# Performance work log

Hardware: AMD Instinct MI355X
Metric: run time of the kernel (lower is better)

Reference implementation:

```python
import jax, jax.numpy as jnp
import numpy as np

B, C, H, W = 2, 192, 128, 128
DG, K = 4, 9  # deformable groups, kernel taps (3x3)


def conv3x3(x, w, b):
    y = jax.lax.conv_general_dilated(x, w, (1, 1), ((1, 1), (1, 1)),
                                     dimension_numbers=('NCHW', 'OIHW', 'NCHW'))
    return y + b[None, :, None, None]


def deform_sample(x, dy, dx, mask):
    # x: [B,C,H,W]; dy,dx,mask: [B,DG,K,H,W]. Returns [B,C,K,H,W] masked bilinear samples.
    b, c, h, w = x.shape
    cg = c // DG
    kk = jnp.arange(K)
    ky = (kk // 3 - 1).astype(x.dtype)  # kernel row offsets {-1,0,1}, pad=1, stride=1
    kx = (kk % 3 - 1).astype(x.dtype)
    ii = jnp.arange(h, dtype=x.dtype)
    jj = jnp.arange(w, dtype=x.dtype)
    py = ii[None, None, None, :, None] + ky[None, None, :, None, None] + dy  # [B,DG,K,H,W]
    px = jj[None, None, None, None, :] + kx[None, None, :, None, None] + dx
    y0 = jnp.floor(py)
    x0 = jnp.floor(px)
    ly = py - y0
    lx = px - x0
    xf = x.reshape(b, DG, cg, h * w)
    out = jnp.zeros((b, DG, cg, K, h, w), dtype=x.dtype)
    corners = [(y0, x0, (1 - ly) * (1 - lx)), (y0, x0 + 1, (1 - ly) * lx),
               (y0 + 1, x0, ly * (1 - lx)), (y0 + 1, x0 + 1, ly * lx)]
    for yc, xc, wt in corners:
        valid = (yc >= 0) & (yc < h) & (xc >= 0) & (xc < w)  # zero padding outside
        wv = wt * valid.astype(x.dtype)
        idx = (jnp.clip(yc, 0, h - 1) * w + jnp.clip(xc, 0, w - 1)).astype(jnp.int32)
        idxb = jnp.broadcast_to(idx.reshape(b, DG, 1, K * h * w), (b, DG, cg, K * h * w))
        g = jnp.take_along_axis(xf, idxb, axis=3).reshape(b, DG, cg, K, h, w)
        out = out + wv[:, :, None] * g
    out = out * mask[:, :, None]
    return out.reshape(b, c, K, h, w)


def setup_inputs() -> dict:
    key = jax.random.key(0)
    ks = jax.random.split(key, 8)
    f32 = jnp.float32
    x_vq = jax.random.normal(ks[0], (B, C, H, W), f32)
    x_residual = jax.random.normal(ks[1], (B, C, H, W), f32)
    w_off = jax.random.normal(ks[2], (C, 2 * C, 3, 3), f32) * (1.0 / np.sqrt(2 * C * 9))
    b_off = jnp.zeros((C,), f32)
    # conv_offset of DCNv2Pack: C -> 3*DG*K channels; small init keeps offsets moderate
    w_co = jax.random.normal(ks[3], (3 * DG * K, C, 3, 3), f32) * 0.02
    b_co = jnp.zeros((3 * DG * K,), f32)
    w_dcn = jax.random.normal(ks[4], (C, C, 3, 3), f32) * (1.0 / np.sqrt(C * 9))
    b_dcn = jnp.zeros((C,), f32)
    return {"x_vq": x_vq, "x_residual": x_residual, "w_off": w_off, "b_off": b_off,
            "w_co": w_co, "b_co": b_co, "w_dcn": w_dcn, "b_dcn": b_dcn}


def reference(x_vq, x_residual, w_off, b_off, w_co, b_co, w_dcn, b_dcn):
    feat = conv3x3(jnp.concatenate([x_vq, x_residual], axis=1), w_off, b_off)  # [B,C,H,W]
    off_out = conv3x3(feat, w_co, b_co)  # [B,3*DG*K,H,W]
    gk = DG * K
    o1 = off_out[:, :gk]
    o2 = off_out[:, gk:2 * gk]
    mask = jax.nn.sigmoid(off_out[:, 2 * gk:])
    dy = o1.reshape(B, DG, K, H, W)
    dx = o2.reshape(B, DG, K, H, W)
    m = mask.reshape(B, DG, K, H, W)
    sampled = deform_sample(x_vq, dy, dx, m)  # [B,C,K,H,W]
    y = jnp.einsum('ock,bckhw->bohw', w_dcn.reshape(C, C, K), sampled)
    return y + b_dcn[None, :, None, None]
```

## Files before the change

### kernel.cpp

```cpp
#include <hip/hip_runtime.h>
#include <hip/hip_bf16.h>
#include <math.h>

#define HH 128
#define WW 128
#define HW 16384
#define BB 2
#define CC 192

typedef __attribute__((ext_vector_type(8)))  short short8;
typedef __attribute__((ext_vector_type(4)))  float f32x4;
typedef __attribute__((ext_vector_type(16))) float f32x16;
typedef __attribute__((ext_vector_type(2)))  float f32x2;
typedef __attribute__((ext_vector_type(4)))  unsigned u32x4;

static __device__ __forceinline__ short f2bf(float f) {
    unsigned u = __float_as_uint(f);
    unsigned r = (u + 0x7FFFu + ((u >> 16) & 1u)) >> 16;
    return (short)r;
}
static __device__ __forceinline__ f32x2 unpk(unsigned u) {
    f32x2 r;
    r[0] = __uint_as_float(u << 16);
    r[1] = __uint_as_float(u & 0xFFFF0000u);
    return r;
}

static __device__ __forceinline__ void gl_lds16(const short* gsrc, short* ldst) {
    __builtin_amdgcn_global_load_lds(
        (const __attribute__((address_space(1))) unsigned*)gsrc,
        (__attribute__((address_space(3))) unsigned*)ldst, 16, 0, 0);
}

__global__ __launch_bounds__(256) void to_grp_k(
    const float* __restrict__ xv, const float* __restrict__ xr,
    unsigned short* __restrict__ xg)
{
    const int idx = blockIdx.x * 256 + threadIdx.x;
    const int pos = idx & (HW - 1);
    const int cgb = idx >> 14;
    const int cg  = cgb % 48;
    const int b   = cgb / 48;
    short8 v;
#pragma unroll
    for (int r = 0; r < 8; r++) {
        const int c = cg * 8 + r;
        const float f = (c < 192)
            ? xv[((size_t)(b * 192 + c) << 14) + pos]
            : xr[((size_t)(b * 192 + (c - 192)) << 14) + pos];
        v[r] = f2bf(f);
    }
    *reinterpret_cast<short8*>(xg + (size_t)idx * 8) = v;
}

__global__ void pack_w_k(const float* __restrict__ w, short* __restrict__ wp,
                         int Co, int so, int d1, int s1, int d2, int s2, int s3,
                         int total)
{
    const int idx = blockIdx.x * blockDim.x + threadIdx.x;
    if (idx >= total) return;
    const int lane  = idx & 63;
    const int slot  = (idx >> 6) & 7;
    const int chunk = idx >> 9;
    const int o     = slot * 32 + (lane & 31);
    const int k0    = chunk * 16 + ((lane >> 5) << 3);
    short8 v;
#pragma unroll
    for (int r = 0; r < 8; r++) {
        const int k = k0 + r;
        float f = 0.f;
        if (o < Co) {
            const int rem = k % d1;
            f = w[(size_t)o * so + (k / d1) * s1 + (rem / d2) * s2 + (rem % d2) * s3];
        }
        v[r] = f2bf(f);
    }
    *reinterpret_cast<short8*>(wp + (size_t)idx * 8) = v;
}

template<int MTW, int NC16, bool OUT_GRP>
__global__ __launch_bounds__(256, 2) void conv_g_k(
    const unsigned short* __restrict__ xg,
    const short* __restrict__ wA, const float* __restrict__ bias,
    void* __restrict__ outp, int Cout)
{
    __shared__ __align__(16) short Pbuf[3][2][4096];

    const int t    = threadIdx.x;
    const int lane = t & 63;
    const int wid  = t >> 6;
    const int mg   = wid >> 1;
    const int nt   = wid & 1;
    const int lin  = (blockIdx.z * HH + blockIdx.y) * 2 + blockIdx.x;
    const int og_  = (lin & 7) * 64 + (lin >> 3);
    const int j0   = (og_ & 1) * 64;
    const int i    = (og_ >> 1) & (HH - 1);
    const int b    = og_ >> 8;
    const int px   = j0 + (nt << 5) + (lane & 31);
    const int hi   = lane >> 5;
    constexpr int NQ = NC16 * 9;
    constexpr int NP = NQ / 2;

    const unsigned short* __restrict__ xgb = xg + (size_t)b * (NC16 * 2) * HW * 8;

    f32x16 acc[MTW];
#pragma unroll
    for (int m = 0; m < MTW; m++)
#pragma unroll
        for (int r = 0; r < 16; r++) acc[m][r] = 0.f;

    auto loadB = [&](int qq, short8& dst, bool& vm) {
        const int c16 = qq / 9;
        const int tap = qq - c16 * 9;
        const int iy  = i + tap / 3 - 1;
        const int jx  = px + tap % 3 - 1;
        vm = ((unsigned)iy < HH) && ((unsigned)jx < WW);
        const int iyc = min(max(iy, 0), HH - 1);
        const int jxc = min(max(jx, 0), WW - 1);
        dst = *reinterpret_cast<const short8*>(
            xgb + ((size_t)(c16 * 2 + hi) * HW + (iyc << 7) + jxc) * 8);
    };
    auto stage2 = [&](int chunk, int pb, int sl) {
        gl_lds16(wA + (size_t)chunk * 4096 + t * 8,         &Pbuf[pb][sl][wid * 512]);
        gl_lds16(wA + (size_t)chunk * 4096 + (t + 256) * 8, &Pbuf[pb][sl][2048 + wid * 512]);
    };

    short8 B0, B1, B2, B3, B4, B5;
    bool M0, M1, M2, M3, M4, M5;

    stage2(0, 0, 0); stage2(1, 0, 1);
    loadB(0, B0, M0); loadB(1, B1, M1);
    stage2(2, 1, 0); stage2(3, 1, 1);
    loadB(2, B2, M2); loadB(3, B3, M3);

#define CCHUNK(IBUF, SL, BC, MC)                                              \
    {                                                                         \
        short8 bF = BC;                                                       \
        if (!MC) {                                                            \
            _Pragma("unroll")                                                 \
            for (int r = 0; r < 8; r++) bF[r] = 0;                            \
        }                                                                     \
        const short* ab_ = &Pbuf[IBUF][SL][(mg * MTW) * 512 + lane * 8];      \
        short8 aF[MTW];                                                       \
        _Pragma("unroll")                                                     \
        for (int m = 0; m < MTW; m++)                                         \
            aF[m] = *reinterpret_cast<const short8*>(ab_ + m * 512);          \
        _Pragma("unroll")                                                     \
        for (int m = 0; m < MTW; m++)                                         \
            acc[m] = __builtin_amdgcn_mfma_f32_32x32x16_bf16(aF[m], bF, acc[m], 0, 0, 0); \
    }

#define PSTEP(P, IBUF, SBUF, Bc0, Mc0, Bc1, Mc1, Bn0, Mn0, Bn1, Mn1)          \
    {                                                                         \
        loadB(min(2 * ((P) + 2),     NQ - 1), Bn0, Mn0);                      \
        loadB(min(2 * ((P) + 2) + 1, NQ - 1), Bn1, Mn1);                      \
        asm volatile("s_waitcnt vmcnt(8)" ::: "memory");                      \
        __builtin_amdgcn_s_barrier();                                         \
        __builtin_amdgcn_sched_barrier(0);                                    \
        const int sc0_ = min(2 * ((P) + 2),     NQ - 1);                      \
        const int sc1_ = min(2 * ((P) + 2) + 1, NQ - 1);                      \
        stage2(sc0_, SBUF, 0); stage2(sc1_, SBUF, 1);                         \
        CCHUNK(IBUF, 0, Bc0, Mc0);                                            \
        CCHUNK(IBUF, 1, Bc1, Mc1);                                            \
    }

    for (int pp = 0; pp < NP; pp += 3) {
        PSTEP(pp + 0, 0, 2, B0, M0, B1, M1, B4, M4, B5, M5);
        PSTEP(pp + 1, 1, 0, B2, M2, B3, M3, B0, M0, B1, M1);
        PSTEP(pp + 2, 2, 1, B4, M4, B5, M5, B2, M2, B3, M3);
    }
#undef PSTEP
#undef CCHUNK

    const int pos_o = (i << 7) + px;
    if constexpr (OUT_GRP) {
        unsigned short* fg = (unsigned short*)outp;
#pragma unroll
        for (int m = 0; m < MTW; m++) {
            const int mt32 = mg * MTW + m;
#pragma unroll
            for (int g = 0; g < 4; g++) {
                const int ob = mt32 * 32 + 8 * g + 4 * hi;
                const unsigned s0 = (unsigned short)f2bf(acc[m][4 * g + 0] + bias[ob + 0]);
                const unsigned s1 = (unsigned short)f2bf(acc[m][4 * g + 1] + bias[ob + 1]);
                const unsigned s2 = (unsigned short)f2bf(acc[m][4 * g + 2] + bias[ob + 2]);
                const unsigned s3 = (unsigned short)f2bf(acc[m][4 * g + 3] + bias[ob + 3]);
                const int cg = mt32 * 4 + g;
                *reinterpret_cast<uint2*>(
                    fg + ((size_t)(b * (Cout >> 3) + cg) * HW + pos_o) * 8 + 4 * hi) =
                    make_uint2(s0 | (s1 << 16), s2 | (s3 << 16));
            }
        }
    } else {
        float* of = (float*)outp;
#pragma unroll
        for (int m = 0; m < MTW; m++) {
            const int mt32 = mg * MTW + m;
#pragma unroll
            for (int reg = 0; reg < 16; reg++) {
                const int o = mt32 * 32 + (reg & 3) + ((reg >> 2) << 3) + (hi << 2);
                if (o < Cout)
                    of[((size_t)(b * Cout + o) << 14) + pos_o] = acc[m][reg] + bias[o];
            }
        }
    }
}

__global__ __launch_bounds__(128, 2) void dcn_g_k(
    const unsigned short* __restrict__ xg, const float* __restrict__ off,
    const short* __restrict__ wA, const float* __restrict__ bias,
    float* __restrict__ out)
{
    __shared__ __align__(16) f32x4 eW[1152];
    __shared__ __align__(8)  uint2 eO[1152];
    __shared__ __align__(16) short bfS[2][2][512];

    const int t    = threadIdx.x;
    const int lane = t & 63;
    const int w    = t >> 6;
    const int lin  = (blockIdx.z * HH + blockIdx.y) * 4 + blockIdx.x;
    const int og_  = (lin & 7) * 128 + (lin >> 3);
    const int jt   = og_ & 3;
    const int i    = (og_ >> 2) & (HH - 1);
    const int b    = og_ >> 9;
    const int j0   = jt * 32;

    for (int e = t; e < 1152; e += 128) {
        const int p  = e & 31;
        const int gk = e >> 5;
        const int kt = gk % 9;
        const int j  = j0 + p;
        const size_t sp = (size_t)b * 108 * HW + (size_t)gk * HW + (i << 7) + j;
        const float dy = off[sp];
        const float dx = off[sp + (size_t)36 * HW];
        const float mv = off[sp + (size_t)72 * HW];
        const float m  = 1.f / (1.f + expf(-mv));
        const float py = (float)(i + kt / 3 - 1) + dy;
        const float px = (float)(j + kt % 3 - 1) + dx;
        const float y0f = floorf(py), x0f = floorf(px);
        const float ly = py - y0f, lx = px - x0f;
        const int y0 = (int)y0f, x0 = (int)x0f;
        const float vy0 = (y0 >= 0 && y0 < HH) ? 1.f : 0.f;
        const float vy1 = (y0 + 1 >= 0 && y0 + 1 < HH) ? 1.f : 0.f;
        const float vx0 = (x0 >= 0 && x0 < WW) ? 1.f : 0.f;
        const float vx1 = (x0 + 1 >= 0 && x0 + 1 < WW) ? 1.f : 0.f;
        f32x4 w4;
        w4[0] = (1.f - ly) * (1.f - lx) * m * vy0 * vx0;
        w4[1] = (1.f - ly) * lx         * m * vy0 * vx1;
        w4[2] = ly         * (1.f - lx) * m * vy1 * vx0;
        w4[3] = ly         * lx         * m * vy1 * vx1;
        const int yc0 = min(max(y0, 0), HH - 1);
        const int yc1 = min(max(y0 + 1, 0), HH - 1);
        const int xc0 = min(max(x0, 0), WW - 1);
        const int xc1 = min(max(x0 + 1, 0), WW - 1);
        eW[e] = w4;
        eO[e] = make_uint2((unsigned)((yc0 << 7) + xc0) | ((unsigned)((yc0 << 7) + xc1) << 16),
                           (unsigned)((yc1 << 7) + xc0) | ((unsigned)((yc1 << 7) + xc1) << 16));
    }
    __syncthreads();

    const int px_l = lane & 31;
    const int hi   = lane >> 5;
    const unsigned short* __restrict__ xgb = xg + (size_t)b * 48 * HW * 8;

    f32x16 acc[3];
#pragma unroll
    for (int m = 0; m < 3; m++)
#pragma unroll
        for (int r = 0; r < 16; r++) acc[m][r] = 0.f;

#define GISSUE(QQ, N0, N1, N2, N3, WN)                                        \
    {                                                                         \
        const int qn_   = min((QQ), 107);                                     \
        const int c16n_ = qn_ / 9;                                            \
        const int ktn_  = qn_ - 9 * c16n_;                                    \
        const int e_    = ((c16n_ / 3) * 9 + ktn_) * 32 + px_l;               \
        const uint2 o_  = eO[e_];                                             \
        WN = eW[e_];                                                          \
        const unsigned short* base_ = xgb + (size_t)(c16n_ * 2 + hi) * (HW * 8); \
        N0 = *reinterpret_cast<const u32x4*>(base_ + (size_t)(o_.x & 0xFFFFu) * 8); \
        N1 = *reinterpret_cast<const u32x4*>(base_ + (size_t)(o_.x >> 16) * 8);     \
        N2 = *reinterpret_cast<const u32x4*>(base_ + (size_t)(o_.y & 0xFFFFu) * 8); \
        N3 = *reinterpret_cast<const u32x4*>(base_ + (size_t)(o_.y >> 16) * 8);     \
    }

#define AISSUE(PP, DST)                                                       \
    {                                                                         \
        const short* a0_ = wA + (size_t)min(2 * (PP),     107) * 4096 + (w * 3) * 512 + lane * 8; \
        const short* a1_ = wA + (size_t)min(2 * (PP) + 1, 107) * 4096 + (w * 3) * 512 + lane * 8; \
        DST[0] = *reinterpret_cast<const short8*>(a0_);                       \
        DST[1] = *reinterpret_cast<const short8*>(a0_ + 512);                 \
        DST[2] = *reinterpret_cast<const short8*>(a0_ + 1024);                \
        DST[3] = *reinterpret_cast<const short8*>(a1_);                       \
        DST[4] = *reinterpret_cast<const short8*>(a1_ + 512);                 \
        DST[5] = *reinterpret_cast<const short8*>(a1_ + 1024);                \
    }

#define PAIRSTEP(P, Ac, C0, C1, C2, C3, WC, An, N0, N1, N2, N3, WN)           \
    {                                                                         \
        GISSUE(2 * ((P) + 1) + w, N0, N1, N2, N3, WN);                        \
        AISSUE((P) + 1, An);                                                  \
        asm volatile("s_waitcnt vmcnt(10)" ::: "memory");                     \
        u32x4 rv_;                                                            \
        _Pragma("unroll")                                                     \
        for (int jj = 0; jj < 4; jj++) {                                      \
            f32x2 v_ = WC[0] * unpk(C0[jj]) + WC[1] * unpk(C1[jj])            \
                     + WC[2] * unpk(C2[jj]) + WC[3] * unpk(C3[jj]);           \
            __hip_bfloat162 h2_ = __float22bfloat162_rn(make_float2(v_[0], v_[1])); \
            unsigned hu_; __builtin_memcpy(&hu_, &h2_, 4);                    \
            rv_[jj] = hu_;                                                    \
        }                                                                     \
        *reinterpret_cast<u32x4*>(&bfS[(P) & 1][w][lane * 8]) = rv_;          \
        asm volatile("s_waitcnt lgkmcnt(0)" ::: "memory");                    \
        __builtin_amdgcn_s_barrier();                                         \
        __builtin_amdgcn_sched_barrier(0);                                    \
        const short8 bf0_ = *reinterpret_cast<const short8*>(&bfS[(P) & 1][0][lane * 8]); \
        const short8 bf1_ = *reinterpret_cast<const short8*>(&bfS[(P) & 1][1][lane * 8]); \
        acc[0] = __builtin_amdgcn_mfma_f32_32x32x16_bf16(Ac[0], bf0_, acc[0], 0, 0, 0); \
        acc[1] = __builtin_amdgcn_mfma_f32_32x32x16_bf16(Ac[1], bf0_, acc[1], 0, 0, 0); \
        acc[2] = __builtin_amdgcn_mfma_f32_32x32x16_bf16(Ac[2], bf0_, acc[2], 0, 0, 0); \
        acc[0] = __builtin_amdgcn_mfma_f32_32x32x16_bf16(Ac[3], bf1_, acc[0], 0, 0, 0); \
        acc[1] = __builtin_amdgcn_mfma_f32_32x32x16_bf16(Ac[4], bf1_, acc[1], 0, 0, 0); \
        acc[2] = __builtin_amdgcn_mfma_f32_32x32x16_bf16(Ac[5], bf1_, acc[2], 0, 0, 0); \
    }

    short8 Aa[6], Ab[6];
    u32x4 Gx0, Gx1, Gx2, Gx3, Gy0, Gy1, Gy2, Gy3;
    f32x4 wGx, wGy;

    GISSUE(0 + w, Gx0, Gx1, Gx2, Gx3, wGx);
    AISSUE(0, Aa);

    for (int pr = 0; pr < 54; pr += 2) {
        PAIRSTEP(pr,     Aa, Gx0, Gx1, Gx2, Gx3, wGx, Ab, Gy0, Gy1, Gy2, Gy3, wGy);
        PAIRSTEP(pr + 1, Ab, Gy0, Gy1, Gy2, Gy3, wGy, Aa, Gx0, Gx1, Gx2, Gx3, wGx);
    }
#undef PAIRSTEP
#undef AISSUE
#undef GISSUE

    const int pos_o = (i << 7) + j0 + px_l;
#pragma unroll
    for (int m = 0; m < 3; m++) {
        const int mt32 = w * 3 + m;
#pragma unroll
        for (int reg = 0; reg < 16; reg++) {
            const int o = mt32 * 32 + (reg & 3) + ((reg >> 2) << 3) + (hi << 2);
            out[((size_t)(b * CC + o) << 14) + pos_o] = acc[m][reg] + bias[o];
        }
    }
}

extern "C" void kernel_launch(void* const* d_in, const int* in_sizes, int n_in,
                              void* d_out, int out_size, void* d_ws, size_t ws_size,
                              hipStream_t stream)
{
    const float* x_vq  = (const float*)d_in[0];
    const float* x_res = (const float*)d_in[1];
    const float* w_off = (const float*)d_in[2];
    const float* b_off = (const float*)d_in[3];
    const float* w_co  = (const float*)d_in[4];
    const float* b_co  = (const float*)d_in[5];
    const float* w_dcn = (const float*)d_in[6];
    const float* b_dcn = (const float*)d_in[7];
    float* out = (float*)d_out;

    char* ws = (char*)d_ws;
    unsigned short* xg = (unsigned short*)ws;
    const size_t xg_sz = (size_t)BB * 48 * HW * 8 * 2;
    unsigned short* fg = (unsigned short*)(ws + xg_sz);
    const size_t fg_sz = (size_t)BB * 24 * HW * 8 * 2;
    float* offb = (float*)(ws + xg_sz + fg_sz);
    const size_t offb_sz = (size_t)BB * 108 * HW * 4;
    short* wA1 = (short*)(ws + xg_sz + fg_sz + offb_sz);
    short* wA2 = wA1 + (size_t)216 * 4096;
    short* wA3 = wA2 + (size_t)108 * 4096;

    to_grp_k<<<dim3(BB * 48 * HW / 256), 256, 0, stream>>>(x_vq, x_res, xg);

    pack_w_k<<<(216 * 512 + 255) / 256, 256, 0, stream>>>(
        w_off, wA1, 192, 3456, 144, 144, 16, 1, 9, 216 * 512);
    pack_w_k<<<(108 * 512 + 255) / 256, 256, 0, stream>>>(
        w_co, wA2, 108, 1728, 144, 144, 16, 1, 9, 108 * 512);
    pack_w_k<<<(108 * 512 + 255) / 256, 256, 0, stream>>>(
        w_dcn, wA3, 192, 1728, 144, 144, 16, 1, 9, 108 * 512);

    conv_g_k<3, 24, true><<<dim3(2, HH, BB), 256, 0, stream>>>(xg, wA1, b_off, fg, 192);
    conv_g_k<2, 12, false><<<dim3(2, HH, BB), 256, 0, stream>>>(fg, wA2, b_co, offb, 108);
    dcn_g_k<<<dim3(4, HH, BB), 128, 0, stream>>>(xg, offb, wA3, b_dcn, out);
}
```

Before: 175.5 us.

## Widen conv tiles to full rows and double DCN block pixel tile

The two implicit-GEMM conv kernels now process a full 128-pixel row per block. Each warp holds two N-subtiles of accumulators, so every LDS-staged weight fragment feeds twice as many MFMAs and the grid is halved. Occupancy drops to one block per CU, and for the MTW=2 conv only half the weight chunk is staged. The DCN kernel moves from 128 to 256 threads and a 64-pixel tile, with warps split into M and N halves that share the gathered bilinear samples and weight loads. This cuts redundant weight traffic but doubles shared memory per block.

```diff
diff --git a/kernel.cpp b/kernel.cpp
--- a/kernel.cpp
+++ b/kernel.cpp
@@ -79,7 +79,7 @@
 }
 
 template<int MTW, int NC16, bool OUT_GRP>
-__global__ __launch_bounds__(256, 2) void conv_g_k(
+__global__ __launch_bounds__(256, 1) void conv_g_k(
     const unsigned short* __restrict__ xg,
     const short* __restrict__ wA, const float* __restrict__ bias,
     void* __restrict__ outp, int Cout)
@@ -91,143 +91,162 @@
     const int wid  = t >> 6;
     const int mg   = wid >> 1;
     const int nt   = wid & 1;
-    const int lin  = (blockIdx.z * HH + blockIdx.y) * 2 + blockIdx.x;
-    const int og_  = (lin & 7) * 64 + (lin >> 3);
-    const int j0   = (og_ & 1) * 64;
-    const int i    = (og_ >> 1) & (HH - 1);
-    const int b    = og_ >> 8;
-    const int px   = j0 + (nt << 5) + (lane & 31);
+    const int lin  = blockIdx.y * HH + blockIdx.x;
+    const int og_  = (lin & 7) * 32 + (lin >> 3);
+    const int i    = og_ & (HH - 1);
+    const int b    = og_ >> 7;
+    const int pxb  = nt * 64 + (lane & 31);
     const int hi   = lane >> 5;
     constexpr int NQ = NC16 * 9;
     constexpr int NP = NQ / 2;
 
     const unsigned short* __restrict__ xgb = xg + (size_t)b * (NC16 * 2) * HW * 8;
 
-    f32x16 acc[MTW];
+    f32x16 acc[MTW][2];
 #pragma unroll
     for (int m = 0; m < MTW; m++)
 #pragma unroll
-        for (int r = 0; r < 16; r++) acc[m][r] = 0.f;
-
-    auto loadB = [&](int qq, short8& dst, bool& vm) {
+        for (int n = 0; n < 2; n++)
+#pragma unroll
+            for (int r = 0; r < 16; r++) acc[m][n][r] = 0.f;
+
+    auto loadB = [&](int qq, int nn, short8& dst, bool& vm) {
         const int c16 = qq / 9;
         const int tap = qq - c16 * 9;
         const int iy  = i + tap / 3 - 1;
-        const int jx  = px + tap % 3 - 1;
+        const int jx  = pxb + nn * 32 + tap % 3 - 1;
         vm = ((unsigned)iy < HH) && ((unsigned)jx < WW);
         const int iyc = min(max(iy, 0), HH - 1);
         const int jxc = min(max(jx, 0), WW - 1);
         dst = *reinterpret_cast<const short8*>(
             xgb + ((size_t)(c16 * 2 + hi) * HW + (iyc << 7) + jxc) * 8);
     };
-    auto stage2 = [&](int chunk, int pb, int sl) {
-        gl_lds16(wA + (size_t)chunk * 4096 + t * 8,         &Pbuf[pb][sl][wid * 512]);
-        gl_lds16(wA + (size_t)chunk * 4096 + (t + 256) * 8, &Pbuf[pb][sl][2048 + wid * 512]);
+    auto stage = [&](int chunk, int pb, int sl) {
+        gl_lds16(wA + (size_t)chunk * 4096 + t * 8, &Pbuf[pb][sl][wid * 512]);
+        if constexpr (MTW >= 3)
+            gl_lds16(wA + (size_t)chunk * 4096 + (t + 256) * 8,
+                     &Pbuf[pb][sl][2048 + wid * 512]);
     };
-
-    short8 B0, B1, B2, B3, B4, B5;
-    bool M0, M1, M2, M3, M4, M5;
-
-    stage2(0, 0, 0); stage2(1, 0, 1);
-    loadB(0, B0, M0); loadB(1, B1, M1);
-    stage2(2, 1, 0); stage2(3, 1, 1);
-    loadB(2, B2, M2); loadB(3, B3, M3);
-
-#define CCHUNK(IBUF, SL, BC, MC)                                              \
+    auto loadB4 = [&](int P, short8* Bset, bool* Mset) {
+        loadB(min(2 * P,     NQ - 1), 0, Bset[0], Mset[0]);
+        loadB(min(2 * P,     NQ - 1), 1, Bset[1], Mset[1]);
+        loadB(min(2 * P + 1, NQ - 1), 0, Bset[2], Mset[2]);
+        loadB(min(2 * P + 1, NQ - 1), 1, Bset[3], Mset[3]);
+    };
+
+    short8 Bs0[4], Bs1[4], Bs2[4];
+    bool   Ms0[4], Ms1[4], Ms2[4];
+
+    stage(0, 0, 0); stage(1, 0, 1);
+    loadB4(0, Bs0, Ms0);
+    stage(2, 1, 0); stage(3, 1, 1);
+    loadB4(1, Bs1, Ms1);
+
+#define CCHUNK(IBUF, SL, Bset, Mset, O)                                       \
     {                                                                         \
-        short8 bF = BC;                                                       \
-        if (!MC) {                                                            \
-            _Pragma("unroll")                                                 \
-            for (int r = 0; r < 8; r++) bF[r] = 0;                            \
-        }                                                                     \
+        short8 bF0 = Bset[(O) + 0];                                           \
+        short8 bF1 = Bset[(O) + 1];                                           \
+        if (!Mset[(O) + 0]) { _Pragma("unroll")                               \
+            for (int r = 0; r < 8; r++) bF0[r] = 0; }                         \
+        if (!Mset[(O) + 1]) { _Pragma("unroll")                               \
+            for (int r = 0; r < 8; r++) bF1[r] = 0; }                         \
         const short* ab_ = &Pbuf[IBUF][SL][(mg * MTW) * 512 + lane * 8];      \
         short8 aF[MTW];                                                       \
         _Pragma("unroll")                                                     \
         for (int m = 0; m < MTW; m++)                                         \
             aF[m] = *reinterpret_cast<const short8*>(ab_ + m * 512);          \
         _Pragma("unroll")                                                     \
-        for (int m = 0; m < MTW; m++)                                         \
-            acc[m] = __builtin_amdgcn_mfma_f32_32x32x16_bf16(aF[m], bF, acc[m], 0, 0, 0); \
-    }
-
-#define PSTEP(P, IBUF, SBUF, Bc0, Mc0, Bc1, Mc1, Bn0, Mn0, Bn1, Mn1)          \
+        for (int m = 0; m < MTW; m++) {                                       \
+            acc[m][0] = __builtin_amdgcn_mfma_f32_32x32x16_bf16(aF[m], bF0, acc[m][0], 0, 0, 0); \
+            acc[m][1] = __builtin_amdgcn_mfma_f32_32x32x16_bf16(aF[m], bF1, acc[m][1], 0, 0, 0); \
+        }                                                                     \
+    }
+
+#define PSTEP(P, IBUF, SBUF, Bc, Mc, Bn, Mn)                                  \
     {                                                                         \
-        loadB(min(2 * ((P) + 2),     NQ - 1), Bn0, Mn0);                      \
-        loadB(min(2 * ((P) + 2) + 1, NQ - 1), Bn1, Mn1);                      \
-        asm volatile("s_waitcnt vmcnt(8)" ::: "memory");                      \
+        loadB4(min((P) + 2, NP - 1), Bn, Mn);                                 \
+        if constexpr (MTW >= 3) {                                             \
+            asm volatile("s_waitcnt vmcnt(12)" ::: "memory");                 \
+        } else {                                                              \
+            asm volatile("s_waitcnt vmcnt(10)" ::: "memory");                 \
+        }                                                                     \
         __builtin_amdgcn_s_barrier();                                         \
         __builtin_amdgcn_sched_barrier(0);                                    \
-        const int sc0_ = min(2 * ((P) + 2),     NQ - 1);                      \
-        const int sc1_ = min(2 * ((P) + 2) + 1, NQ - 1);                      \
-        stage2(sc0_, SBUF, 0); stage2(sc1_, SBUF, 1);                         \
-        CCHUNK(IBUF, 0, Bc0, Mc0);                                            \
-        CCHUNK(IBUF, 1, Bc1, Mc1);                                            \
+        const int p2_ = min((P) + 2, NP - 1);                                 \
+        stage(min(2 * p2_,     NQ - 1), SBUF, 0);                             \
+        stage(min(2 * p2_ + 1, NQ - 1), SBUF, 1);                             \
+        CCHUNK(IBUF, 0, Bc, Mc, 0);                                           \
+        CCHUNK(IBUF, 1, Bc, Mc, 2);                                           \
     }
 
     for (int pp = 0; pp < NP; pp += 3) {
-        PSTEP(pp + 0, 0, 2, B0, M0, B1, M1, B4, M4, B5, M5);
-        PSTEP(pp + 1, 1, 0, B2, M2, B3, M3, B0, M0, B1, M1);
-        PSTEP(pp + 2, 2, 1, B4, M4, B5, M5, B2, M2, B3, M3);
+        PSTEP(pp + 0, 0, 2, Bs0, Ms0, Bs2, Ms2);
+        PSTEP(pp + 1, 1, 0, Bs1, Ms1, Bs0, Ms0);
+        PSTEP(pp + 2, 2, 1, Bs2, Ms2, Bs1, Ms1);
     }
 #undef PSTEP
 #undef CCHUNK
 
-    const int pos_o = (i << 7) + px;
-    if constexpr (OUT_GRP) {
-        unsigned short* fg = (unsigned short*)outp;
-#pragma unroll
-        for (int m = 0; m < MTW; m++) {
-            const int mt32 = mg * MTW + m;
-#pragma unroll
-            for (int g = 0; g < 4; g++) {
-                const int ob = mt32 * 32 + 8 * g + 4 * hi;
-                const unsigned s0 = (unsigned short)f2bf(acc[m][4 * g + 0] + bias[ob + 0]);
-                const unsigned s1 = (unsigned short)f2bf(acc[m][4 * g + 1] + bias[ob + 1]);
-                const unsigned s2 = (unsigned short)f2bf(acc[m][4 * g + 2] + bias[ob + 2]);
-                const unsigned s3 = (unsigned short)f2bf(acc[m][4 * g + 3] + bias[ob + 3]);
-                const int cg = mt32 * 4 + g;
-                *reinterpret_cast<uint2*>(
-                    fg + ((size_t)(b * (Cout >> 3) + cg) * HW + pos_o) * 8 + 4 * hi) =
-                    make_uint2(s0 | (s1 << 16), s2 | (s3 << 16));
+#pragma unroll
+    for (int nn = 0; nn < 2; nn++) {
+        const int pos_o = (i << 7) + pxb + nn * 32;
+        if constexpr (OUT_GRP) {
+            unsigned short* fg = (unsigned short*)outp;
+#pragma unroll
+            for (int m = 0; m < MTW; m++) {
+                const int mt32 = mg * MTW + m;
+#pragma unroll
+                for (int g = 0; g < 4; g++) {
+                    const int ob = mt32 * 32 + 8 * g + 4 * hi;
+                    const unsigned s0 = (unsigned short)f2bf(acc[m][nn][4 * g + 0] + bias[ob + 0]);
+                    const unsigned s1 = (unsigned short)f2bf(acc[m][nn][4 * g + 1] + bias[ob + 1]);
+                    const unsigned s2 = (unsigned short)f2bf(acc[m][nn][4 * g + 2] + bias[ob + 2]);
+                    const unsigned s3 = (unsigned short)f2bf(acc[m][nn][4 * g + 3] + bias[ob + 3]);
+                    const int cg = mt32 * 4 + g;
+                    *reinterpret_cast<uint2*>(
+                        fg + ((size_t)(b * (Cout >> 3) + cg) * HW + pos_o) * 8 + 4 * hi) =
+                        make_uint2(s0 | (s1 << 16), s2 | (s3 << 16));
+                }
+            }
+        } else {
+            float* of = (float*)outp;
+#pragma unroll
+            for (int m = 0; m < MTW; m++) {
+                const int mt32 = mg * MTW + m;
+#pragma unroll
+                for (int reg = 0; reg < 16; reg++) {
+                    const int o = mt32 * 32 + (reg & 3) + ((reg >> 2) << 3) + (hi << 2);
+                    if (o < Cout)
+                        of[((size_t)(b * Cout + o) << 14) + pos_o] = acc[m][nn][reg] + bias[o];
+                }
             }
         }
-    } else {
-        float* of = (float*)outp;
-#pragma unroll
-        for (int m = 0; m < MTW; m++) {
-            const int mt32 = mg * MTW + m;
-#pragma unroll
-            for (int reg = 0; reg < 16; reg++) {
-                const int o = mt32 * 32 + (reg & 3) + ((reg >> 2) << 3) + (hi << 2);
-                if (o < Cout)
-                    of[((size_t)(b * Cout + o) << 14) + pos_o] = acc[m][reg] + bias[o];
-            }
-        }
-    }
-}
-
-__global__ __launch_bounds__(128, 2) void dcn_g_k(
+    }
+}
+
+__global__ __launch_bounds__(256, 2) void dcn_g_k(
     const unsigned short* __restrict__ xg, const float* __restrict__ off,
     const short* __restrict__ wA, const float* __restrict__ bias,
     float* __restrict__ out)
 {
-    __shared__ __align__(16) f32x4 eW[1152];
-    __shared__ __align__(8)  uint2 eO[1152];
-    __shared__ __align__(16) short bfS[2][2][512];
+    __shared__ __align__(16) f32x4 eW[2304];
+    __shared__ __align__(8)  uint2 eO[2304];
+    __shared__ __align__(16) short bfS[2][2][2][512];
 
     const int t    = threadIdx.x;
     const int lane = t & 63;
-    const int w    = t >> 6;
-    const int lin  = (blockIdx.z * HH + blockIdx.y) * 4 + blockIdx.x;
-    const int og_  = (lin & 7) * 128 + (lin >> 3);
-    const int jt   = og_ & 3;
-    const int i    = (og_ >> 2) & (HH - 1);
-    const int b    = og_ >> 9;
-    const int j0   = jt * 32;
-
-    for (int e = t; e < 1152; e += 128) {
-        const int p  = e & 31;
-        const int gk = e >> 5;
+    const int wid  = t >> 6;
+    const int nh   = wid >> 1;
+    const int mh   = wid & 1;
+    const int lin  = (blockIdx.z * HH + blockIdx.y) * 2 + blockIdx.x;
+    const int og_  = (lin & 7) * 64 + (lin >> 3);
+    const int j0   = (og_ & 1) * 64;
+    const int i    = (og_ >> 1) & (HH - 1);
+    const int b    = og_ >> 8;
+
+    for (int e = t; e < 2304; e += 256) {
+        const int p  = e & 63;
+        const int gk = e >> 6;
         const int kt = gk % 9;
         const int j  = j0 + p;
         const size_t sp = (size_t)b * 108 * HW + (size_t)gk * HW + (i << 7) + j;
@@ -259,7 +278,7 @@
     }
     __syncthreads();
 
-    const int px_l = lane & 31;
+    const int px_a = nh * 32 + (lane & 31);
     const int hi   = lane >> 5;
     const unsigned short* __restrict__ xgb = xg + (size_t)b * 48 * HW * 8;
 
@@ -274,7 +293,7 @@
         const int qn_   = min((QQ), 107);                                     \
         const int c16n_ = qn_ / 9;                                            \
         const int ktn_  = qn_ - 9 * c16n_;                                    \
-        const int e_    = ((c16n_ / 3) * 9 + ktn_) * 32 + px_l;               \
+        const int e_    = ((c16n_ / 3) * 9 + ktn_) * 64 + px_a;               \
         const uint2 o_  = eO[e_];                                             \
         WN = eW[e_];                                                          \
         const unsigned short* base_ = xgb + (size_t)(c16n_ * 2 + hi) * (HW * 8); \
@@ -286,8 +305,8 @@
 
 #define AISSUE(PP, DST)                                                       \
     {                                                                         \
-        const short* a0_ = wA + (size_t)min(2 * (PP),     107) * 4096 + (w * 3) * 512 + lane * 8; \
-        const short* a1_ = wA + (size_t)min(2 * (PP) + 1, 107) * 4096 + (w * 3) * 512 + lane * 8; \
+        const short* a0_ = wA + (size_t)min(2 * (PP),     107) * 4096 + (mh * 3) * 512 + lane * 8; \
+        const short* a1_ = wA + (size_t)min(2 * (PP) + 1, 107) * 4096 + (mh * 3) * 512 + lane * 8; \
         DST[0] = *reinterpret_cast<const short8*>(a0_);                       \
         DST[1] = *reinterpret_cast<const short8*>(a0_ + 512);                 \
         DST[2] = *reinterpret_cast<const short8*>(a0_ + 1024);                \
@@ -298,7 +317,7 @@
 
 #define PAIRSTEP(P, Ac, C0, C1, C2, C3, WC, An, N0, N1, N2, N3, WN)           \
     {                                                                         \
-        GISSUE(2 * ((P) + 1) + w, N0, N1, N2, N3, WN);                        \
+        GISSUE(2 * ((P) + 1) + mh, N0, N1, N2, N3, WN);                       \
         AISSUE((P) + 1, An);                                                  \
         asm volatile("s_waitcnt vmcnt(10)" ::: "memory");                     \
         u32x4 rv_;                                                            \
@@ -310,12 +329,12 @@
             unsigned hu_; __builtin_memcpy(&hu_, &h2_, 4);                    \
             rv_[jj] = hu_;                                                    \
         }                                                                     \
-        *reinterpret_cast<u32x4*>(&bfS[(P) & 1][w][lane * 8]) = rv_;          \
+        *reinterpret_cast<u32x4*>(&bfS[(P) & 1][mh][nh][lane * 8]) = rv_;     \
         asm volatile("s_waitcnt lgkmcnt(0)" ::: "memory");                    \
         __builtin_amdgcn_s_barrier();                                         \
         __builtin_amdgcn_sched_barrier(0);                                    \
-        const short8 bf0_ = *reinterpret_cast<const short8*>(&bfS[(P) & 1][0][lane * 8]); \
-        const short8 bf1_ = *reinterpret_cast<const short8*>(&bfS[(P) & 1][1][lane * 8]); \
+        const short8 bf0_ = *reinterpret_cast<const short8*>(&bfS[(P) & 1][0][nh][lane * 8]); \
+        const short8 bf1_ = *reinterpret_cast<const short8*>(&bfS[(P) & 1][1][nh][lane * 8]); \
         acc[0] = __builtin_amdgcn_mfma_f32_32x32x16_bf16(Ac[0], bf0_, acc[0], 0, 0, 0); \
         acc[1] = __builtin_amdgcn_mfma_f32_32x32x16_bf16(Ac[1], bf0_, acc[1], 0, 0, 0); \
         acc[2] = __builtin_amdgcn_mfma_f32_32x32x16_bf16(Ac[2], bf0_, acc[2], 0, 0, 0); \
@@ -328,7 +347,7 @@
     u32x4 Gx0, Gx1, Gx2, Gx3, Gy0, Gy1, Gy2, Gy3;
     f32x4 wGx, wGy;
 
-    GISSUE(0 + w, Gx0, Gx1, Gx2, Gx3, wGx);
+    GISSUE(0 + mh, Gx0, Gx1, Gx2, Gx3, wGx);
     AISSUE(0, Aa);
 
     for (int pr = 0; pr < 54; pr += 2) {
@@ -339,10 +358,10 @@
 #undef AISSUE
 #undef GISSUE
 
-    const int pos_o = (i << 7) + j0 + px_l;
+    const int pos_o = (i << 7) + j0 + px_a;
 #pragma unroll
     for (int m = 0; m < 3; m++) {
-        const int mt32 = w * 3 + m;
+        const int mt32 = mh * 3 + m;
 #pragma unroll
         for (int reg = 0; reg < 16; reg++) {
             const int o = mt32 * 32 + (reg & 3) + ((reg >> 2) << 3) + (hi << 2);
@@ -385,7 +404,7 @@
     pack_w_k<<<(108 * 512 + 255) / 256, 256, 0, stream>>>(
         w_dcn, wA3, 192, 1728, 144, 144, 16, 1, 9, 108 * 512);
 
-    conv_g_k<3, 24, true><<<dim3(2, HH, BB), 256, 0, stream>>>(xg, wA1, b_off, fg, 192);
-    conv_g_k<2, 12, false><<<dim3(2, HH, BB), 256, 0, stream>>>(fg, wA2, b_co, offb, 108);
-    dcn_g_k<<<dim3(4, HH, BB), 128, 0, stream>>>(xg, offb, wA3, b_dcn, out);
-}
+    conv_g_k<3, 24, true><<<dim3(HH, BB), 256, 0, stream>>>(xg, wA1, b_off, fg, 192);
+    conv_g_k<2, 12, false><<<dim3(HH, BB), 256, 0, stream>>>(fg, wA2, b_co, offb, 108);
+    dcn_g_k<<<dim3(2, HH, BB), 256, 0, stream>>>(xg, offb, wA3, b_dcn, out);
+}
```

After: 185.0 us. 5.4% more time.

## Restructure conv pipeline to double-buffered four-chunk stages

Applied to the files above, without the earlier changes.

Replaces the triple-buffered two-chunk software pipeline in the implicit-GEMM conv kernel with a double-buffered scheme that stages four weight chunks and four B-fragment loads per step. Each step issues one barrier per four MFMA chunks instead of one per two, which cuts synchronisation overhead and gives more independent loads in flight. The stage helper skips the second weight-copy half when MTW is below 3. In exchange, prefetch depth falls from two steps ahead to one, and more B fragments stay live in registers. The min-clamped indices also add some redundant loads on the final partial step.

```diff
diff --git a/kernel.cpp b/kernel.cpp
--- a/kernel.cpp
+++ b/kernel.cpp
@@ -84,7 +84,7 @@
     const short* __restrict__ wA, const float* __restrict__ bias,
     void* __restrict__ outp, int Cout)
 {
-    __shared__ __align__(16) short Pbuf[3][2][4096];
+    __shared__ __align__(16) short Pbuf[2][4][4096];
 
     const int t    = threadIdx.x;
     const int lane = t & 63;
@@ -99,7 +99,7 @@
     const int px   = j0 + (nt << 5) + (lane & 31);
     const int hi   = lane >> 5;
     constexpr int NQ = NC16 * 9;
-    constexpr int NP = NQ / 2;
+    constexpr int NS = NQ / 4;
 
     const unsigned short* __restrict__ xgb = xg + (size_t)b * (NC16 * 2) * HW * 8;
 
@@ -120,27 +120,40 @@
         dst = *reinterpret_cast<const short8*>(
             xgb + ((size_t)(c16 * 2 + hi) * HW + (iyc << 7) + jxc) * 8);
     };
-    auto stage2 = [&](int chunk, int pb, int sl) {
-        gl_lds16(wA + (size_t)chunk * 4096 + t * 8,         &Pbuf[pb][sl][wid * 512]);
-        gl_lds16(wA + (size_t)chunk * 4096 + (t + 256) * 8, &Pbuf[pb][sl][2048 + wid * 512]);
+    auto stage = [&](int chunk, int buf, int sl) {
+        gl_lds16(wA + (size_t)chunk * 4096 + t * 8, &Pbuf[buf][sl][wid * 512]);
+        if constexpr (MTW >= 3)
+            gl_lds16(wA + (size_t)chunk * 4096 + (t + 256) * 8,
+                     &Pbuf[buf][sl][2048 + wid * 512]);
     };
 
-    short8 B0, B1, B2, B3, B4, B5;
-    bool M0, M1, M2, M3, M4, M5;
-
-    stage2(0, 0, 0); stage2(1, 0, 1);
-    loadB(0, B0, M0); loadB(1, B1, M1);
-    stage2(2, 1, 0); stage2(3, 1, 1);
-    loadB(2, B2, M2); loadB(3, B3, M3);
-
-#define CCHUNK(IBUF, SL, BC, MC)                                              \
-    {                                                                         \
-        short8 bF = BC;                                                       \
-        if (!MC) {                                                            \
-            _Pragma("unroll")                                                 \
-            for (int r = 0; r < 8; r++) bF[r] = 0;                            \
-        }                                                                     \
-        const short* ab_ = &Pbuf[IBUF][SL][(mg * MTW) * 512 + lane * 8];      \
+#define LOADB4(P, Bset, Mset)                                                 \
+    {                                                                         \
+        loadB(min(4 * (P) + 0, NQ - 1), Bset[0], Mset[0]);                    \
+        loadB(min(4 * (P) + 1, NQ - 1), Bset[1], Mset[1]);                    \
+        loadB(min(4 * (P) + 2, NQ - 1), Bset[2], Mset[2]);                    \
+        loadB(min(4 * (P) + 3, NQ - 1), Bset[3], Mset[3]);                    \
+    }
+#define STAGE4(P, BUFI)                                                       \
+    {                                                                         \
+        stage(min(4 * (P) + 0, NQ - 1), BUFI, 0);                             \
+        stage(min(4 * (P) + 1, NQ - 1), BUFI, 1);                             \
+        stage(min(4 * (P) + 2, NQ - 1), BUFI, 2);                             \
+        stage(min(4 * (P) + 3, NQ - 1), BUFI, 3);                             \
+    }
+
+    short8 Bs0[4], Bs1[4];
+    bool   Ms0[4], Ms1[4];
+
+    STAGE4(0, 0);
+    LOADB4(0, Bs0, Ms0);
+
+#define CCHUNK4(BUFI, C, Bset, Mset)                                          \
+    {                                                                         \
+        short8 bF = Bset[C];                                                  \
+        if (!Mset[C]) { _Pragma("unroll")                                     \
+            for (int r = 0; r < 8; r++) bF[r] = 0; }                          \
+        const short* ab_ = &Pbuf[BUFI][C][(mg * MTW) * 512 + lane * 8];       \
         short8 aF[MTW];                                                       \
         _Pragma("unroll")                                                     \
         for (int m = 0; m < MTW; m++)                                         \
@@ -150,27 +163,28 @@
             acc[m] = __builtin_amdgcn_mfma_f32_32x32x16_bf16(aF[m], bF, acc[m], 0, 0, 0); \
     }
 
-#define PSTEP(P, IBUF, SBUF, Bc0, Mc0, Bc1, Mc1, Bn0, Mn0, Bn1, Mn1)          \
-    {                                                                         \
-        loadB(min(2 * ((P) + 2),     NQ - 1), Bn0, Mn0);                      \
-        loadB(min(2 * ((P) + 2) + 1, NQ - 1), Bn1, Mn1);                      \
-        asm volatile("s_waitcnt vmcnt(8)" ::: "memory");                      \
+#define SSTEP(P, BUFI, Bc, Mc, Bn, Mn)                                        \
+    {                                                                         \
+        const int pn_ = min((P) + 1, NS - 1);                                 \
+        LOADB4(pn_, Bn, Mn);                                                  \
+        asm volatile("s_waitcnt vmcnt(4)" ::: "memory");                      \
         __builtin_amdgcn_s_barrier();                                         \
         __builtin_amdgcn_sched_barrier(0);                                    \
-        const int sc0_ = min(2 * ((P) + 2),     NQ - 1);                      \
-        const int sc1_ = min(2 * ((P) + 2) + 1, NQ - 1);                      \
-        stage2(sc0_, SBUF, 0); stage2(sc1_, SBUF, 1);                         \
-        CCHUNK(IBUF, 0, Bc0, Mc0);                                            \
-        CCHUNK(IBUF, 1, Bc1, Mc1);                                            \
-    }
-
-    for (int pp = 0; pp < NP; pp += 3) {
-        PSTEP(pp + 0, 0, 2, B0, M0, B1, M1, B4, M4, B5, M5);
-        PSTEP(pp + 1, 1, 0, B2, M2, B3, M3, B0, M0, B1, M1);
-        PSTEP(pp + 2, 2, 1, B4, M4, B5, M5, B2, M2, B3, M3);
-    }
-#undef PSTEP
-#undef CCHUNK
+        STAGE4(pn_, (BUFI) ^ 1);                                              \
+        CCHUNK4(BUFI, 0, Bc, Mc);                                             \
+        CCHUNK4(BUFI, 1, Bc, Mc);                                             \
+        CCHUNK4(BUFI, 2, Bc, Mc);                                             \
+        CCHUNK4(BUFI, 3, Bc, Mc);                                             \
+    }
+
+    for (int pp = 0; pp < NS; pp += 2) {
+        SSTEP(pp, 0, Bs0, Ms0, Bs1, Ms1);
+        if (pp + 1 < NS) SSTEP(pp + 1, 1, Bs1, Ms1, Bs0, Ms0);
+    }
+#undef SSTEP
+#undef CCHUNK4
+#undef STAGE4
+#undef LOADB4
 
     const int pos_o = (i << 7) + px;
     if constexpr (OUT_GRP) {
```

New measurement: 176.1 us. About the same (+0.3%).
